# Kernel tuning notes

Hardware: AMD Instinct MI355X
Metric: run time of the kernel (lower is better)

## Reference

```python
import jax, jax.numpy as jnp
import numpy as np

B, N, D = 2, 1024, 1024
H = 4
KD = 512          # key_dim = d_model * 0.5
VD = 1024         # value_dim = d_model
DK = KD // H      # 128 head_qk_dim
DV = VD // H      # 256 head_v_dim
LR = 16           # gate_low_rank_dim
GLN = 16.0        # gate_logit_normalizer
EPS = 1e-5


def setup_inputs() -> dict:
    key = jax.random.key(0)
    ks = jax.random.split(key, 10)
    s = 0.02
    return {
        "x": jax.random.normal(ks[0], (B, N, D), jnp.float32),
        "Wq": jax.random.normal(ks[1], (D, KD), jnp.float32) * s,
        "Wk": jax.random.normal(ks[2], (D, KD), jnp.float32) * s,
        "Wv": jax.random.normal(ks[3], (D, VD), jnp.float32) * s,
        "Wg": jax.random.normal(ks[4], (D, VD), jnp.float32) * s,
        "Wgk1": jax.random.normal(ks[5], (D, LR), jnp.float32) * s,
        "Wgk2": jax.random.normal(ks[6], (LR, KD), jnp.float32) * s,
        "bgk2": jax.random.normal(ks[7], (KD,), jnp.float32) * s,
        "Wout": jax.random.normal(ks[8], (VD, D), jnp.float32) * s,
        "rms_w": jnp.ones((DV,), jnp.float32),
    }


def _split_heads(t, h):
    b, n, hd = t.shape
    return t.reshape(b, n, h, hd // h).transpose(0, 2, 1, 3)  # b h n d


def _gla_scan(q, k, v, g):
    # q,k: [b,h,n,dk]; v: [b,h,n,dv]; g: [b,h,n,dk] (log-decay)
    b, h, n, dk = q.shape
    dv = v.shape[-1]
    qT = jnp.moveaxis(q, 2, 0)  # [n,b,h,dk]
    kT = jnp.moveaxis(k, 2, 0)
    vT = jnp.moveaxis(v, 2, 0)
    gT = jnp.moveaxis(g, 2, 0)

    def step(S, inp):
        qt, kt, vt, gt = inp
        # S_t = diag(exp(g_t)) S_{t-1} + k_t v_t^T ; o_t = q_t S_t
        S = S * jnp.exp(gt)[..., None] + kt[..., None] * vt[..., None, :]
        ot = jnp.einsum('bhk,bhkv->bhv', qt, S)
        return S, ot

    S0 = jnp.zeros((b, h, dk, dv), q.dtype)
    _, o = jax.lax.scan(step, S0, (qT, kT, vT, gT))
    return jnp.moveaxis(o, 0, 2)  # [b,h,n,dv]


def reference(x, Wq, Wk, Wv, Wg, Wgk1, Wgk2, bgk2, Wout, rms_w):
    q = _split_heads(x @ Wq, H)
    k = _split_heads(x @ Wk, H)
    v = _split_heads(x @ Wv, H)
    g = jax.nn.log_sigmoid((x @ Wgk1) @ Wgk2 + bgk2) / GLN
    g = jnp.maximum(g, -3.0)  # chunk mode clamp
    g = _split_heads(g, H)
    o = _gla_scan(q, k, v, g)               # [b,h,n,dv]
    o = o.transpose(0, 2, 1, 3)             # [b,n,h,dv]
    # RMSNorm over head_v_dim
    o = o * jax.lax.rsqrt(jnp.mean(o * o, axis=-1, keepdims=True) + EPS) * rms_w
    o = o.reshape(o.shape[0], o.shape[1], VD)
    o = o * jax.nn.silu(x @ Wg)
    return o @ Wout
```

## Files before the change

kernel.cpp:

```cpp
#include <hip/hip_runtime.h>
#include <math.h>


typedef __attribute__((ext_vector_type(4))) float vf4;
typedef __attribute__((ext_vector_type(2))) float vf2;
typedef __attribute__((ext_vector_type(4))) unsigned int vu4;
typedef __attribute__((ext_vector_type(8))) short short8;
typedef __attribute__((ext_vector_type(4))) unsigned short us4;

#define DEVI static __device__ __forceinline__
DEVI vf4 vzero() { vf4 x = {0.f, 0.f, 0.f, 0.f}; return x; }

DEVI float bf2f(unsigned int u) {
  union { unsigned int i; float f; } c; c.i = u << 16; return c.f;
}
DEVI unsigned short f2bf(float f) {
  union { float f; unsigned int i; } c; c.f = f;
  unsigned int i = c.i;
  return (unsigned short)((i + 0x7fffu + ((i >> 16) & 1u)) >> 16);
}
DEVI void unpack8(vu4 r, float* f) {
  f[0] = bf2f(r.x & 0xffffu); f[1] = bf2f(r.x >> 16);
  f[2] = bf2f(r.y & 0xffffu); f[3] = bf2f(r.y >> 16);
  f[4] = bf2f(r.z & 0xffffu); f[5] = bf2f(r.z >> 16);
  f[6] = bf2f(r.w & 0xffffu); f[7] = bf2f(r.w >> 16);
}
DEVI vu4 pack8(const float* f) {
  vu4 o;
  o.x = (unsigned int)f2bf(f[0]) | ((unsigned int)f2bf(f[1]) << 16);
  o.y = (unsigned int)f2bf(f[2]) | ((unsigned int)f2bf(f[3]) << 16);
  o.z = (unsigned int)f2bf(f[4]) | ((unsigned int)f2bf(f[5]) << 16);
  o.w = (unsigned int)f2bf(f[6]) | ((unsigned int)f2bf(f[7]) << 16);
  return o;
}

DEVI void gld16(const unsigned short* g, unsigned short* l) {
  __builtin_amdgcn_global_load_lds(
      (const __attribute__((address_space(1))) unsigned int*)g,
      (__attribute__((address_space(3))) unsigned int*)l,
      16, 0, 0);
}

__global__ __launch_bounds__(256)
void wtrans_k(const float* __restrict__ Wq, const float* __restrict__ Wk,
              const float* __restrict__ Wv, const float* __restrict__ Wg,
              const float* __restrict__ Wo,
              unsigned short* __restrict__ wqT, unsigned short* __restrict__ wkT,
              unsigned short* __restrict__ wvT, unsigned short* __restrict__ wgT,
              unsigned short* __restrict__ woT) {
  __shared__ float T[2][64][65];
  const int t = threadIdx.x;
  const int r = t >> 2, s = t & 3;
  float f[2][16];
  const float* srcs[2];
  unsigned short* dsts[2];
#pragma unroll
  for (int i = 0; i < 2; ++i) {
    const int tid = blockIdx.x * 2 + i;
    const float* W; unsigned short* O; int kt, cb, N;
    if (tid < 128)       { W = Wq; O = wqT; N = 512;  kt = tid >> 3;          cb = tid & 7;  }
    else if (tid < 256)  { W = Wk; O = wkT; N = 512;  kt = (tid - 128) >> 3;  cb = tid & 7;  }
    else if (tid < 512)  { W = Wv; O = wvT; N = 1024; kt = (tid - 256) >> 4;  cb = tid & 15; }
    else if (tid < 768)  { W = Wg; O = wgT; N = 1024; kt = (tid - 512) >> 4;  cb = tid & 15; }
    else                 { W = Wo; O = woT; N = 1024; kt = (tid - 768) >> 4;  cb = tid & 15; }
    srcs[i] = W + (size_t)(kt * 64 + r) * N + cb * 64 + s * 16;
    dsts[i] = O + (size_t)(cb * 64 + r) * 1024 + kt * 64 + s * 16;
  }
#pragma unroll
  for (int i = 0; i < 2; ++i)
#pragma unroll
    for (int u = 0; u < 4; ++u)
      *(vf4*)&f[i][u * 4] = *(const vf4*)(srcs[i] + u * 4);
#pragma unroll
  for (int i = 0; i < 2; ++i)
#pragma unroll
    for (int u = 0; u < 16; ++u)
      T[i][r][s * 16 + u] = f[i][u];
  __syncthreads();
#pragma unroll
  for (int i = 0; i < 2; ++i) {
    unsigned int pk[8];
#pragma unroll
    for (int u = 0; u < 8; ++u) {
      unsigned int lo = f2bf(T[i][s * 16 + 2 * u][r]);
      unsigned int hi = f2bf(T[i][s * 16 + 2 * u + 1][r]);
      pk[u] = lo | (hi << 16);
    }
    *(vu4*)dsts[i] = *(vu4*)&pk[0];
    *(vu4*)(dsts[i] + 8) = *(vu4*)&pk[4];
  }
}

__global__ __launch_bounds__(256)
void xcvt_lr_k(const float* __restrict__ X, const float* __restrict__ Wgk1,
               unsigned short* __restrict__ xb, float* __restrict__ xl) {
  const int bid = blockIdx.x, t = threadIdx.x;
  if (bid < 512) {
    const size_t base = (size_t)bid * 4096 + t * 16;
    float f[16];
    *(vf4*)&f[0]  = *(const vf4*)(X + base);
    *(vf4*)&f[4]  = *(const vf4*)(X + base + 4);
    *(vf4*)&f[8]  = *(const vf4*)(X + base + 8);
    *(vf4*)&f[12] = *(const vf4*)(X + base + 12);
    *(vu4*)(xb + base) = pack8(f);
    *(vu4*)(xb + base + 8) = pack8(f + 8);
    return;
  }
  const int w = t >> 6, lane = t & 63;
  const int row = (bid - 512) * 4 + w;
  float acc[16];
#pragma unroll
  for (int c2 = 0; c2 < 16; ++c2) acc[c2] = 0.f;
  const float* xp = X + (size_t)row * 1024 + lane * 16;
  float xv[16];
#pragma unroll
  for (int u = 0; u < 4; ++u)
    *(vf4*)&xv[u * 4] = *(const vf4*)(xp + u * 4);
#pragma unroll
  for (int j = 0; j < 16; ++j) {
    const float* wp = Wgk1 + (size_t)(lane * 16 + j) * 16;
    float wv[16];
#pragma unroll
    for (int u = 0; u < 4; ++u)
      *(vf4*)&wv[u * 4] = *(const vf4*)(wp + u * 4);
#pragma unroll
    for (int c2 = 0; c2 < 16; ++c2) acc[c2] = fmaf(xv[j], wv[c2], acc[c2]);
  }
#pragma unroll
  for (int mm = 1; mm < 64; mm <<= 1) {
#pragma unroll
    for (int c2 = 0; c2 < 16; ++c2) acc[c2] += __shfl_xor(acc[c2], mm, 64);
  }
  if (lane == 0) {
#pragma unroll
    for (int c2 = 0; c2 < 16; ++c2) xl[(size_t)row * 16 + c2] = acc[c2];
  }
}

__global__ __launch_bounds__(256)
void proj_mfma_k(const unsigned short* __restrict__ xb,
                 const unsigned short* __restrict__ wqT, const unsigned short* __restrict__ wkT,
                 const unsigned short* __restrict__ wvT, const unsigned short* __restrict__ wgT,
                 unsigned short* __restrict__ qb, unsigned short* __restrict__ kb,
                 unsigned short* __restrict__ vb, unsigned short* __restrict__ sgb) {
  __shared__ __align__(16) unsigned short As[128 * 64];
  __shared__ __align__(16) unsigned short Bs[128 * 64];
  const int t = threadIdx.x;
  const int m0 = blockIdx.y << 7;
  const int nt = blockIdx.x;
  const unsigned short* WT; int n0; int kind;
  if (nt < 4)       { WT = wqT; n0 = nt << 7;        kind = 0; }
  else if (nt < 8)  { WT = wkT; n0 = (nt - 4) << 7;  kind = 1; }
  else if (nt < 16) { WT = wvT; n0 = (nt - 8) << 7;  kind = 2; }
  else              { WT = wgT; n0 = (nt - 16) << 7; kind = 3; }

  const int w = t >> 6, lane = t & 63;
  const int wm = (w >> 1) << 6, wn = (w & 1) << 6;
  const int qd = lane >> 4, m = lane & 15;
  const int srow = lane >> 3;
  const int scol = ((lane & 7) ^ srow) << 3;

  vf4 acc[4][4];
#pragma unroll
  for (int i = 0; i < 4; ++i)
#pragma unroll
    for (int j = 0; j < 4; ++j) acc[i][j] = vzero();

  for (int k0 = 0; k0 < 1024; k0 += 64) {
    __syncthreads();
#pragma unroll
    for (int cc = 0; cc < 4; ++cc) {
      const int c = (w << 2) + cc;
      const int row = (c << 3) + srow;
      gld16(xb + (size_t)(m0 + row) * 1024 + k0 + scol, (unsigned short*)As + (c << 9));
      gld16(WT + (size_t)(n0 + row) * 1024 + k0 + scol, (unsigned short*)Bs + (c << 9));
    }
    __syncthreads();
#pragma unroll
    for (int ks = 0; ks < 2; ++ks) {
      const int sw = (((ks << 2) + qd) ^ (m & 7)) << 3;
      short8 af[4], bf[4];
#pragma unroll
      for (int i = 0; i < 4; ++i)
        af[i] = *(const short8*)&As[(wm + i * 16 + m) * 64 + sw];
#pragma unroll
      for (int j = 0; j < 4; ++j)
        bf[j] = *(const short8*)&Bs[(wn + j * 16 + m) * 64 + sw];
#pragma unroll
      for (int i = 0; i < 4; ++i)
#pragma unroll
        for (int j = 0; j < 4; ++j)
          acc[i][j] = __builtin_amdgcn_mfma_f32_16x16x32_bf16(af[i], bf[j], acc[i][j], 0, 0, 0);
    }
  }
#pragma unroll
  for (int i = 0; i < 4; ++i) {
#pragma unroll
    for (int j = 0; j < 4; ++j) {
#pragma unroll
      for (int r = 0; r < 4; ++r) {
        const int grow = m0 + wm + i * 16 + qd * 4 + r;
        const int gcol = n0 + wn + j * 16 + m;
        float val = acc[i][j][r];
        if (kind == 0)      qb[(size_t)grow * 512 + gcol] = f2bf(val);
        else if (kind == 1) kb[(size_t)grow * 512 + gcol] = f2bf(val);
        else if (kind == 2) vb[(size_t)grow * 1024 + gcol] = f2bf(val);
        else {
          val = val / (1.f + expf(-val));
          sgb[(size_t)grow * 1024 + gcol] = f2bf(val);
        }
      }
    }
  }
}

__global__ __launch_bounds__(256)
void gate_scan_k(const float* __restrict__ xl, const float* __restrict__ W2,
                 const float* __restrict__ bias,
                 unsigned short* __restrict__ q, unsigned short* __restrict__ k,
                 float* __restrict__ ebtot) {
  const int t = threadIdx.x;
  const int w = t >> 6, lane = t & 63;
  const int wid = blockIdx.x * 4 + w;
  const int kt = wid & 31;
  const int c = (wid >> 5) & 15;
  const int b = wid >> 9;
  const int kbase = kt * 16;
  const size_t rowbase = (size_t)b * 1024 + c * 64;

  const float* xp = xl + (rowbase + lane) * 16;
  float xv[16];
#pragma unroll
  for (int u = 0; u < 4; ++u)
    *(vf4*)&xv[u * 4] = *(const vf4*)(xp + u * 4);

  const size_t a = (rowbase + lane) * 512 + kbase;
  vu4 qr0 = *(const vu4*)(q + a), qr1 = *(const vu4*)(q + a + 8);
  vu4 kr0 = *(const vu4*)(k + a), kr1 = *(const vu4*)(k + a + 8);
  float qf[16], kf[16];
  unpack8(qr0, qf); unpack8(qr1, qf + 8);
  unpack8(kr0, kf); unpack8(kr1, kf + 8);

  float gf[16];
#pragma unroll
  for (int cc = 0; cc < 16; ++cc) {
    const int col = kbase + cc;
    float z = bias[col];
#pragma unroll
    for (int j = 0; j < 16; ++j) z = fmaf(xv[j], W2[j * 512 + col], z);
    float ls = fminf(z, 0.f) - log1pf(expf(-fabsf(z)));
    float g = fmaxf(ls * (1.f / 16.f), -3.f);
#pragma unroll
    for (int d = 1; d < 64; d <<= 1) {
      float up = __shfl_up(g, d, 64);
      if (lane >= d) g += up;
    }
    qf[cc] *= expf(g);
    kf[cc] *= expf(fminf(-g, 80.f));
    gf[cc] = g;
  }
  *(vu4*)(q + a) = pack8(qf);
  *(vu4*)(q + a + 8) = pack8(qf + 8);
  *(vu4*)(k + a) = pack8(kf);
  *(vu4*)(k + a + 8) = pack8(kf + 8);
  if (lane == 63) {
    float* ep = ebtot + ((size_t)b * 16 + c) * 512 + kbase;
#pragma unroll
    for (int cc = 0; cc < 16; ++cc) ep[cc] = expf(gf[cc]);
  }
}

__global__ __launch_bounds__(256)
void intra_kv_k(const unsigned short* __restrict__ q16, const unsigned short* __restrict__ k16,
                const unsigned short* __restrict__ v, float* __restrict__ o,
                unsigned short* __restrict__ ST) {
  __shared__ __align__(16) unsigned short Qs[64 * 136];
  __shared__ __align__(16) unsigned short Ks[64 * 136];
  __shared__ __align__(16) unsigned short Kt[128 * 68];
  __shared__ __align__(16) unsigned short Vt[128 * 68];
  __shared__ __align__(16) unsigned short Asb[64 * 68];
  const int t = threadIdx.x;
  const int vh = blockIdx.x, c = blockIdx.y, bh = blockIdx.z;
  const int b = bh >> 2, h = bh & 3;
  const size_t rowbase = (size_t)b * 1024 + c * 64;

#pragma unroll
  for (int u2 = 0; u2 < 4; ++u2) {
    const int id = t + (u2 << 8);
    const int row = id >> 4, kg = id & 15;
    vu4 rq = *(const vu4*)(q16 + (rowbase + row) * 512 + h * 128 + kg * 8);
    *(vu4*)&Qs[row * 136 + kg * 8] = rq;
    vu4 rk = *(const vu4*)(k16 + (rowbase + row) * 512 + h * 128 + kg * 8);
    *(vu4*)&Ks[row * 136 + kg * 8] = rk;
    const unsigned short* kp = (const unsigned short*)&rk;
#pragma unroll
    for (int u = 0; u < 8; ++u)
      Kt[(kg * 8 + u) * 68 + row] = kp[u];
    vu4 rv = *(const vu4*)(v + (rowbase + row) * 1024 + h * 256 + vh * 128 + kg * 8);
    const unsigned short* vp = (const unsigned short*)&rv;
#pragma unroll
    for (int u = 0; u < 8; ++u)
      Vt[(kg * 8 + u) * 68 + row] = vp[u];
  }
  __syncthreads();

  const int w = t >> 6, lane = t & 63;
  const int qd = lane >> 4, m = lane & 15;

  {
    short8 af[4];
#pragma unroll
    for (int kf = 0; kf < 4; ++kf)
      af[kf] = *(const short8*)&Qs[(w * 16 + m) * 136 + kf * 32 + qd * 8];
    vf4 acc[4];
#pragma unroll
    for (int jt = 0; jt < 4; ++jt) acc[jt] = vzero();
#pragma unroll
    for (int jt = 0; jt < 4; ++jt)
#pragma unroll
      for (int kf = 0; kf < 4; ++kf) {
        short8 bfr = *(const short8*)&Ks[(jt * 16 + m) * 136 + kf * 32 + qd * 8];
        acc[jt] = __builtin_amdgcn_mfma_f32_16x16x32_bf16(af[kf], bfr, acc[jt], 0, 0, 0);
      }
#pragma unroll
    for (int jt = 0; jt < 4; ++jt)
#pragma unroll
      for (int r = 0; r < 4; ++r) {
        const int i = w * 16 + qd * 4 + r;
        const int j = jt * 16 + m;
        Asb[i * 68 + j] = f2bf((j <= i) ? acc[jt][r] : 0.f);
      }
  }
  __syncthreads();

  {
    vf4 acc2[4][2];
#pragma unroll
    for (int mt = 0; mt < 4; ++mt) { acc2[mt][0] = vzero(); acc2[mt][1] = vzero(); }
#pragma unroll
    for (int kf = 0; kf < 2; ++kf) {
      short8 bf0 = *(const short8*)&Vt[(w * 32 + m) * 68 + kf * 32 + qd * 8];
      short8 bf1 = *(const short8*)&Vt[(w * 32 + 16 + m) * 68 + kf * 32 + qd * 8];
#pragma unroll
      for (int mt = 0; mt < 4; ++mt) {
        short8 af = *(const short8*)&Asb[(mt * 16 + m) * 68 + kf * 32 + qd * 8];
        acc2[mt][0] = __builtin_amdgcn_mfma_f32_16x16x32_bf16(af, bf0, acc2[mt][0], 0, 0, 0);
        acc2[mt][1] = __builtin_amdgcn_mfma_f32_16x16x32_bf16(af, bf1, acc2[mt][1], 0, 0, 0);
      }
    }
#pragma unroll
    for (int mt = 0; mt < 4; ++mt)
#pragma unroll
      for (int nt = 0; nt < 2; ++nt)
#pragma unroll
        for (int r = 0; r < 4; ++r) {
          const int i = mt * 16 + qd * 4 + r;
          const int vc = h * 256 + vh * 128 + w * 32 + nt * 16 + m;
          o[(rowbase + i) * 1024 + vc] = acc2[mt][nt][r];
        }
  }

  {
    short8 af3[2][2];
#pragma unroll
    for (int mt = 0; mt < 2; ++mt)
#pragma unroll
      for (int kf = 0; kf < 2; ++kf)
        af3[mt][kf] = *(const short8*)&Vt[(w * 32 + mt * 16 + m) * 68 + kf * 32 + qd * 8];
#pragma unroll
    for (int nt = 0; nt < 8; ++nt) {
      vf4 a0 = vzero(), a1 = vzero();
#pragma unroll
      for (int kf = 0; kf < 2; ++kf) {
        short8 bfr = *(const short8*)&Kt[(nt * 16 + m) * 68 + kf * 32 + qd * 8];
        a0 = __builtin_amdgcn_mfma_f32_16x16x32_bf16(af3[0][kf], bfr, a0, 0, 0, 0);
        a1 = __builtin_amdgcn_mfma_f32_16x16x32_bf16(af3[1][kf], bfr, a1, 0, 0, 0);
      }
      const size_t sbase = (size_t)(bh * 16 + c) * 256 + vh * 128 + w * 32;
#pragma unroll
      for (int r = 0; r < 4; ++r) {
        ST[(sbase + qd * 4 + r) * 128 + nt * 16 + m] = f2bf(a0[r]);
        ST[(sbase + 16 + qd * 4 + r) * 128 + nt * 16 + m] = f2bf(a1[r]);
      }
    }
  }
}

__global__ __launch_bounds__(256)
void state_scan_k(unsigned short* __restrict__ ST, const float* __restrict__ ebtot) {
  const int idx = blockIdx.x * 256 + threadIdx.x;
  const int kgp = idx & 63;
  const int vv = (idx >> 6) & 255;
  const int bh = idx >> 14;
  const int b = bh >> 2, h = bh & 3;
  const size_t pbase = (size_t)bh * (16 * 256 * 128) + (size_t)vv * 128 + kgp * 2;
  const size_t ebase = (size_t)b * (16 * 512) + h * 128 + kgp * 2;

  unsigned int stv[16];
  vf2 ebv[16];
#pragma unroll
  for (int c = 0; c < 16; ++c) {
    stv[c] = *(const unsigned int*)(ST + pbase + (size_t)c * 32768);
    ebv[c] = *(const vf2*)(ebtot + ebase + (size_t)c * 512);
  }
  float s0 = 0.f, s1 = 0.f;
#pragma unroll
  for (int c = 0; c < 16; ++c) {
    const float kv0 = bf2f(stv[c] & 0xffffu);
    const float kv1 = bf2f(stv[c] >> 16);
    const unsigned int outw =
        (unsigned int)f2bf(s0) | ((unsigned int)f2bf(s1) << 16);
    *(unsigned int*)(ST + pbase + (size_t)c * 32768) = outw;
    s0 = (s0 + kv0) * ebv[c].x;
    s1 = (s1 + kv1) * ebv[c].y;
  }
}

__global__ __launch_bounds__(256)
void o_inter_k(const unsigned short* __restrict__ q16, const unsigned short* __restrict__ ST,
               float* __restrict__ o) {
  __shared__ __align__(16) unsigned short Qs[64 * 136];
  __shared__ __align__(16) unsigned short Ss[128 * 136];
  const int t = threadIdx.x;
  const int vt = blockIdx.x, c = blockIdx.y, bh = blockIdx.z;
  const int b = bh >> 2, h = bh & 3;
  const size_t rowbase = (size_t)b * 1024 + c * 64;

#pragma unroll
  for (int u2 = 0; u2 < 4; ++u2) {
    const int id = t + (u2 << 8);
    const int row = id >> 4, kg = id & 15;
    *(vu4*)&Qs[row * 136 + kg * 8] =
        *(const vu4*)(q16 + (rowbase + row) * 512 + h * 128 + kg * 8);
  }
#pragma unroll
  for (int u2 = 0; u2 < 8; ++u2) {
    const int id = t + (u2 << 8);
    const int vrow = id >> 4, kg = id & 15;
    *(vu4*)&Ss[vrow * 136 + kg * 8] =
        *(const vu4*)(ST + ((size_t)(bh * 16 + c) * 256 + vt * 128 + vrow) * 128 + kg * 8);
  }
  __syncthreads();

  const int w = t >> 6, lane = t & 63;
  const int qd = lane >> 4, m = lane & 15;
  short8 af[4];
#pragma unroll
  for (int kf = 0; kf < 4; ++kf)
    af[kf] = *(const short8*)&Qs[(w * 16 + m) * 136 + kf * 32 + qd * 8];
#pragma unroll
  for (int nt = 0; nt < 8; ++nt) {
    vf4 acc = vzero();
#pragma unroll
    for (int kf = 0; kf < 4; ++kf) {
      short8 bfr = *(const short8*)&Ss[(nt * 16 + m) * 136 + kf * 32 + qd * 8];
      acc = __builtin_amdgcn_mfma_f32_16x16x32_bf16(af[kf], bfr, acc, 0, 0, 0);
    }
    float* base = o + (rowbase + w * 16 + qd * 4) * 1024 + h * 256 + vt * 128 + nt * 16 + m;
#pragma unroll
    for (int r = 0; r < 4; ++r)
      base[(size_t)r * 1024] += acc[r];
  }
}

__global__ __launch_bounds__(256)
void norm_gate_k(const float* __restrict__ o, const float* __restrict__ rmsw,
                 const unsigned short* __restrict__ sg,
                 unsigned short* __restrict__ ob) {
  const int t = threadIdx.x;
  const int w = t >> 6, lane = t & 63;
  const int grp = blockIdx.x * 4 + w;
  const int row = grp >> 2, h = grp & 3;
  const size_t base = (size_t)row * 1024 + h * 256 + lane * 4;
  vf4 val = *(const vf4*)(o + base);
  float ss = val.x * val.x + val.y * val.y + val.z * val.z + val.w * val.w;
#pragma unroll
  for (int mm = 1; mm < 64; mm <<= 1) ss += __shfl_xor(ss, mm, 64);
  const float scale = rsqrtf(ss * (1.f / 256.f) + 1e-5f);
  us4 sgv = *(const us4*)(sg + base);
  vf4 rw = *(const vf4*)(rmsw + lane * 4);
  us4 outv;
  outv.x = f2bf(val.x * scale * rw.x * bf2f((unsigned int)sgv.x));
  outv.y = f2bf(val.y * scale * rw.y * bf2f((unsigned int)sgv.y));
  outv.z = f2bf(val.z * scale * rw.z * bf2f((unsigned int)sgv.z));
  outv.w = f2bf(val.w * scale * rw.w * bf2f((unsigned int)sgv.w));
  *(us4*)(ob + base) = outv;
}

__global__ __launch_bounds__(256)
void out_mfma_k(const unsigned short* __restrict__ Ab,
                const unsigned short* __restrict__ woT, float* __restrict__ Y) {
  __shared__ __align__(16) unsigned short As[64 * 64];
  __shared__ __align__(16) unsigned short Bs[128 * 64];
  const int t = threadIdx.x;
  const int m0 = blockIdx.y << 6;
  const int n0 = blockIdx.x << 7;
  const int w = t >> 6, lane = t & 63;
  const int wm = (w >> 1) * 32, wn = (w & 1) * 64;
  const int qd = lane >> 4, m = lane & 15;
  const int srow = lane >> 3;
  const int scol = ((lane & 7) ^ srow) << 3;

  vf4 acc[2][4];
#pragma unroll
  for (int i = 0; i < 2; ++i)
#pragma unroll
    for (int j = 0; j < 4; ++j) acc[i][j] = vzero();

  for (int k0 = 0; k0 < 1024; k0 += 64) {
    __syncthreads();
#pragma unroll
    for (int cc = 0; cc < 2; ++cc) {
      const int c = (w << 1) + cc;
      const int row = (c << 3) + srow;
      gld16(Ab + (size_t)(m0 + row) * 1024 + k0 + scol, (unsigned short*)As + (c << 9));
    }
#pragma unroll
    for (int cc = 0; cc < 4; ++cc) {
      const int c = (w << 2) + cc;
      const int row = (c << 3) + srow;
      gld16(woT + (size_t)(n0 + row) * 1024 + k0 + scol, (unsigned short*)Bs + (c << 9));
    }
    __syncthreads();
#pragma unroll
    for (int ks = 0; ks < 2; ++ks) {
      const int sw = (((ks << 2) + qd) ^ (m & 7)) << 3;
      short8 af[2], bf[4];
#pragma unroll
      for (int i = 0; i < 2; ++i)
        af[i] = *(const short8*)&As[(wm + i * 16 + m) * 64 + sw];
#pragma unroll
      for (int j = 0; j < 4; ++j)
        bf[j] = *(const short8*)&Bs[(wn + j * 16 + m) * 64 + sw];
#pragma unroll
      for (int i = 0; i < 2; ++i)
#pragma unroll
        for (int j = 0; j < 4; ++j)
          acc[i][j] = __builtin_amdgcn_mfma_f32_16x16x32_bf16(af[i], bf[j], acc[i][j], 0, 0, 0);
    }
  }
#pragma unroll
  for (int i = 0; i < 2; ++i)
#pragma unroll
    for (int j = 0; j < 4; ++j)
#pragma unroll
      for (int r = 0; r < 4; ++r) {
        const int grow = m0 + wm + i * 16 + qd * 4 + r;
        const int gcol = n0 + wn + j * 16 + m;
        Y[(size_t)grow * 1024 + gcol] = acc[i][j][r];
      }
}

extern "C" void kernel_launch(void* const* d_in, const int* in_sizes, int n_in,
                              void* d_out, int out_size, void* d_ws, size_t ws_size,
                              hipStream_t stream) {
  const float* x    = (const float*)d_in[0];
  const float* Wq   = (const float*)d_in[1];
  const float* Wk   = (const float*)d_in[2];
  const float* Wv   = (const float*)d_in[3];
  const float* Wg   = (const float*)d_in[4];
  const float* Wgk1 = (const float*)d_in[5];
  const float* Wgk2 = (const float*)d_in[6];
  const float* bgk2 = (const float*)d_in[7];
  const float* Wout = (const float*)d_in[8];
  const float* rmsw = (const float*)d_in[9];

  const size_t MB = 1u << 20;
  char* w = (char*)d_ws;
  unsigned short* qb16   = (unsigned short*)(w);
  unsigned short* kb16   = (unsigned short*)(w + 2 * MB);
  unsigned short* vbuf   = (unsigned short*)(w + 4 * MB);
  unsigned short* sgbuf  = (unsigned short*)(w + 8 * MB);
  float*          obuf   = (float*)(w + 12 * MB);
  char*           sreg   = w + 20 * MB;
  unsigned short* xb     = (unsigned short*)sreg;
  unsigned short* STbuf  = (unsigned short*)sreg;
  unsigned short* obuf_b = (unsigned short*)sreg;
  float*          xlbuf  = (float*)(w + 28 * MB);
  float*          ebbuf  = (float*)(w + 28 * MB + 131072);
  unsigned short* wqT    = (unsigned short*)(w + 29 * MB);
  unsigned short* wkT    = (unsigned short*)(w + 30 * MB);
  unsigned short* wvT    = (unsigned short*)(w + 31 * MB);
  unsigned short* wgT    = (unsigned short*)(w + 33 * MB);
  unsigned short* woT    = (unsigned short*)(w + 35 * MB);

  wtrans_k<<<512, 256, 0, stream>>>(Wq, Wk, Wv, Wg, Wout, wqT, wkT, wvT, wgT, woT);
  xcvt_lr_k<<<1024, 256, 0, stream>>>(x, Wgk1, xb, xlbuf);
  proj_mfma_k<<<dim3(24, 16), 256, 0, stream>>>(xb, wqT, wkT, wvT, wgT, qb16, kb16, vbuf, sgbuf);
  gate_scan_k<<<256, 256, 0, stream>>>(xlbuf, Wgk2, bgk2, qb16, kb16, ebbuf);
  intra_kv_k<<<dim3(2, 16, 8), 256, 0, stream>>>(qb16, kb16, vbuf, obuf, STbuf);
  state_scan_k<<<512, 256, 0, stream>>>(STbuf, ebbuf);
  o_inter_k<<<dim3(2, 16, 8), 256, 0, stream>>>(qb16, STbuf, obuf);
  norm_gate_k<<<2048, 256, 0, stream>>>(obuf, rmsw, sgbuf, obuf_b);
  out_mfma_k<<<dim3(8, 32), 256, 0, stream>>>(obuf_b, woT, (float*)d_out);
}
```

Measured before the change: 187.5 us.

## Fuse gate computation into chunk kernels and merge prep launches

Merges the weight-transpose and x-convert/low-rank kernels into a single prep launch. Removes the separate gate_scan kernel by recomputing the gate cumsum and q/k scaling inside intra_kv_k and o_inter_k, so scaled q/k no longer round-trip through global memory. The cost is redundant gate computation: each intra block (two v-halves) and each o_inter block recompute log-sigmoid, the prefix scan and exp per column. This trades two launches and one memory pass for extra ALU work.

Result: slower. 209.0 us (+11.5%).

```diff
diff --git a/kernel.cpp b/kernel.cpp
--- a/kernel.cpp
+++ b/kernel.cpp
@@ -41,22 +41,86 @@
       16, 0, 0);
 }
 
+DEVI float gate_g(const float* xv, const float* __restrict__ W2,
+                  const float* __restrict__ bias, int col, int lane) {
+  float z = bias[col];
+#pragma unroll
+  for (int j = 0; j < 16; ++j) z = fmaf(xv[j], W2[j * 512 + col], z);
+  float ls = fminf(z, 0.f) - log1pf(expf(-fabsf(z)));
+  float g = fmaxf(ls * (1.f / 16.f), -3.f);
+#pragma unroll
+  for (int d = 1; d < 64; d <<= 1) {
+    float up = __shfl_up(g, d, 64);
+    if (lane >= d) g += up;
+  }
+  return g;
+}
+
 __global__ __launch_bounds__(256)
-void wtrans_k(const float* __restrict__ Wq, const float* __restrict__ Wk,
-              const float* __restrict__ Wv, const float* __restrict__ Wg,
-              const float* __restrict__ Wo,
-              unsigned short* __restrict__ wqT, unsigned short* __restrict__ wkT,
-              unsigned short* __restrict__ wvT, unsigned short* __restrict__ wgT,
-              unsigned short* __restrict__ woT) {
+void prep_k(const float* __restrict__ Wq, const float* __restrict__ Wk,
+            const float* __restrict__ Wv, const float* __restrict__ Wg,
+            const float* __restrict__ Wo, const float* __restrict__ X,
+            const float* __restrict__ Wgk1,
+            unsigned short* __restrict__ wqT, unsigned short* __restrict__ wkT,
+            unsigned short* __restrict__ wvT, unsigned short* __restrict__ wgT,
+            unsigned short* __restrict__ woT, unsigned short* __restrict__ xb,
+            float* __restrict__ xl) {
   __shared__ float T[2][64][65];
+  const int bid = blockIdx.x;
   const int t = threadIdx.x;
+
+  if (bid >= 1024) {
+    const int w = t >> 6, lane = t & 63;
+    const int row = (bid - 1024) * 4 + w;
+    float acc[16];
+#pragma unroll
+    for (int c2 = 0; c2 < 16; ++c2) acc[c2] = 0.f;
+    const float* xp = X + (size_t)row * 1024 + lane * 16;
+    float xv[16];
+#pragma unroll
+    for (int u = 0; u < 4; ++u)
+      *(vf4*)&xv[u * 4] = *(const vf4*)(xp + u * 4);
+#pragma unroll
+    for (int j = 0; j < 16; ++j) {
+      const float* wp = Wgk1 + (size_t)(lane * 16 + j) * 16;
+      float wv[16];
+#pragma unroll
+      for (int u = 0; u < 4; ++u)
+        *(vf4*)&wv[u * 4] = *(const vf4*)(wp + u * 4);
+#pragma unroll
+      for (int c2 = 0; c2 < 16; ++c2) acc[c2] = fmaf(xv[j], wv[c2], acc[c2]);
+    }
+#pragma unroll
+    for (int mm = 1; mm < 64; mm <<= 1) {
+#pragma unroll
+      for (int c2 = 0; c2 < 16; ++c2) acc[c2] += __shfl_xor(acc[c2], mm, 64);
+    }
+    if (lane == 0) {
+#pragma unroll
+      for (int c2 = 0; c2 < 16; ++c2) xl[(size_t)row * 16 + c2] = acc[c2];
+    }
+    return;
+  }
+
+  if (bid >= 512) {
+    const size_t base = (size_t)(bid - 512) * 4096 + t * 16;
+    float f[16];
+    *(vf4*)&f[0]  = *(const vf4*)(X + base);
+    *(vf4*)&f[4]  = *(const vf4*)(X + base + 4);
+    *(vf4*)&f[8]  = *(const vf4*)(X + base + 8);
+    *(vf4*)&f[12] = *(const vf4*)(X + base + 12);
+    *(vu4*)(xb + base) = pack8(f);
+    *(vu4*)(xb + base + 8) = pack8(f + 8);
+    return;
+  }
+
   const int r = t >> 2, s = t & 3;
   float f[2][16];
   const float* srcs[2];
   unsigned short* dsts[2];
 #pragma unroll
   for (int i = 0; i < 2; ++i) {
-    const int tid = blockIdx.x * 2 + i;
+    const int tid = bid * 2 + i;
     const float* W; unsigned short* O; int kt, cb, N;
     if (tid < 128)       { W = Wq; O = wqT; N = 512;  kt = tid >> 3;          cb = tid & 7;  }
     else if (tid < 256)  { W = Wk; O = wkT; N = 512;  kt = (tid - 128) >> 3;  cb = tid & 7;  }
@@ -88,52 +152,6 @@
     }
     *(vu4*)dsts[i] = *(vu4*)&pk[0];
     *(vu4*)(dsts[i] + 8) = *(vu4*)&pk[4];
-  }
-}
-
-__global__ __launch_bounds__(256)
-void xcvt_lr_k(const float* __restrict__ X, const float* __restrict__ Wgk1,
-               unsigned short* __restrict__ xb, float* __restrict__ xl) {
-  const int bid = blockIdx.x, t = threadIdx.x;
-  if (bid < 512) {
-    const size_t base = (size_t)bid * 4096 + t * 16;
-    float f[16];
-    *(vf4*)&f[0]  = *(const vf4*)(X + base);
-    *(vf4*)&f[4]  = *(const vf4*)(X + base + 4);
-    *(vf4*)&f[8]  = *(const vf4*)(X + base + 8);
-    *(vf4*)&f[12] = *(const vf4*)(X + base + 12);
-    *(vu4*)(xb + base) = pack8(f);
-    *(vu4*)(xb + base + 8) = pack8(f + 8);
-    return;
-  }
-  const int w = t >> 6, lane = t & 63;
-  const int row = (bid - 512) * 4 + w;
-  float acc[16];
-#pragma unroll
-  for (int c2 = 0; c2 < 16; ++c2) acc[c2] = 0.f;
-  const float* xp = X + (size_t)row * 1024 + lane * 16;
-  float xv[16];
-#pragma unroll
-  for (int u = 0; u < 4; ++u)
-    *(vf4*)&xv[u * 4] = *(const vf4*)(xp + u * 4);
-#pragma unroll
-  for (int j = 0; j < 16; ++j) {
-    const float* wp = Wgk1 + (size_t)(lane * 16 + j) * 16;
-    float wv[16];
-#pragma unroll
-    for (int u = 0; u < 4; ++u)
-      *(vf4*)&wv[u * 4] = *(const vf4*)(wp + u * 4);
-#pragma unroll
-    for (int c2 = 0; c2 < 16; ++c2) acc[c2] = fmaf(xv[j], wv[c2], acc[c2]);
-  }
-#pragma unroll
-  for (int mm = 1; mm < 64; mm <<= 1) {
-#pragma unroll
-    for (int c2 = 0; c2 < 16; ++c2) acc[c2] += __shfl_xor(acc[c2], mm, 64);
-  }
-  if (lane == 0) {
-#pragma unroll
-    for (int c2 = 0; c2 < 16; ++c2) xl[(size_t)row * 16 + c2] = acc[c2];
   }
 }
 
@@ -215,65 +233,11 @@
 }
 
 __global__ __launch_bounds__(256)
-void gate_scan_k(const float* __restrict__ xl, const float* __restrict__ W2,
-                 const float* __restrict__ bias,
-                 unsigned short* __restrict__ q, unsigned short* __restrict__ k,
-                 float* __restrict__ ebtot) {
-  const int t = threadIdx.x;
-  const int w = t >> 6, lane = t & 63;
-  const int wid = blockIdx.x * 4 + w;
-  const int kt = wid & 31;
-  const int c = (wid >> 5) & 15;
-  const int b = wid >> 9;
-  const int kbase = kt * 16;
-  const size_t rowbase = (size_t)b * 1024 + c * 64;
-
-  const float* xp = xl + (rowbase + lane) * 16;
-  float xv[16];
-#pragma unroll
-  for (int u = 0; u < 4; ++u)
-    *(vf4*)&xv[u * 4] = *(const vf4*)(xp + u * 4);
-
-  const size_t a = (rowbase + lane) * 512 + kbase;
-  vu4 qr0 = *(const vu4*)(q + a), qr1 = *(const vu4*)(q + a + 8);
-  vu4 kr0 = *(const vu4*)(k + a), kr1 = *(const vu4*)(k + a + 8);
-  float qf[16], kf[16];
-  unpack8(qr0, qf); unpack8(qr1, qf + 8);
-  unpack8(kr0, kf); unpack8(kr1, kf + 8);
-
-  float gf[16];
-#pragma unroll
-  for (int cc = 0; cc < 16; ++cc) {
-    const int col = kbase + cc;
-    float z = bias[col];
-#pragma unroll
-    for (int j = 0; j < 16; ++j) z = fmaf(xv[j], W2[j * 512 + col], z);
-    float ls = fminf(z, 0.f) - log1pf(expf(-fabsf(z)));
-    float g = fmaxf(ls * (1.f / 16.f), -3.f);
-#pragma unroll
-    for (int d = 1; d < 64; d <<= 1) {
-      float up = __shfl_up(g, d, 64);
-      if (lane >= d) g += up;
-    }
-    qf[cc] *= expf(g);
-    kf[cc] *= expf(fminf(-g, 80.f));
-    gf[cc] = g;
-  }
-  *(vu4*)(q + a) = pack8(qf);
-  *(vu4*)(q + a + 8) = pack8(qf + 8);
-  *(vu4*)(k + a) = pack8(kf);
-  *(vu4*)(k + a + 8) = pack8(kf + 8);
-  if (lane == 63) {
-    float* ep = ebtot + ((size_t)b * 16 + c) * 512 + kbase;
-#pragma unroll
-    for (int cc = 0; cc < 16; ++cc) ep[cc] = expf(gf[cc]);
-  }
-}
-
-__global__ __launch_bounds__(256)
-void intra_kv_k(const unsigned short* __restrict__ q16, const unsigned short* __restrict__ k16,
+void intra_kv_k(const float* __restrict__ xl, const float* __restrict__ W2,
+                const float* __restrict__ bias,
+                const unsigned short* __restrict__ q16, const unsigned short* __restrict__ k16,
                 const unsigned short* __restrict__ v, float* __restrict__ o,
-                unsigned short* __restrict__ ST) {
+                unsigned short* __restrict__ ST, float* __restrict__ ebtot) {
   __shared__ __align__(16) unsigned short Qs[64 * 136];
   __shared__ __align__(16) unsigned short Ks[64 * 136];
   __shared__ __align__(16) unsigned short Kt[128 * 68];
@@ -283,29 +247,61 @@
   const int vh = blockIdx.x, c = blockIdx.y, bh = blockIdx.z;
   const int b = bh >> 2, h = bh & 3;
   const size_t rowbase = (size_t)b * 1024 + c * 64;
+  const int w = t >> 6, lane = t & 63;
+  const int qd = lane >> 4, m = lane & 15;
 
 #pragma unroll
   for (int u2 = 0; u2 < 4; ++u2) {
     const int id = t + (u2 << 8);
     const int row = id >> 4, kg = id & 15;
-    vu4 rq = *(const vu4*)(q16 + (rowbase + row) * 512 + h * 128 + kg * 8);
-    *(vu4*)&Qs[row * 136 + kg * 8] = rq;
-    vu4 rk = *(const vu4*)(k16 + (rowbase + row) * 512 + h * 128 + kg * 8);
-    *(vu4*)&Ks[row * 136 + kg * 8] = rk;
-    const unsigned short* kp = (const unsigned short*)&rk;
-#pragma unroll
-    for (int u = 0; u < 8; ++u)
-      Kt[(kg * 8 + u) * 68 + row] = kp[u];
     vu4 rv = *(const vu4*)(v + (rowbase + row) * 1024 + h * 256 + vh * 128 + kg * 8);
     const unsigned short* vp = (const unsigned short*)&rv;
 #pragma unroll
     for (int u = 0; u < 8; ++u)
       Vt[(kg * 8 + u) * 68 + row] = vp[u];
   }
+
+  {
+    const float* xp = xl + (rowbase + lane) * 16;
+    float xv[16];
+#pragma unroll
+    for (int u = 0; u < 4; ++u)
+      *(vf4*)&xv[u * 4] = *(const vf4*)(xp + u * 4);
+    const size_t qa = (rowbase + lane) * 512 + h * 128 + w * 32;
+    vu4 rq[4], rk[4];
+#pragma unroll
+    for (int g8 = 0; g8 < 4; ++g8) {
+      rq[g8] = *(const vu4*)(q16 + qa + g8 * 8);
+      rk[g8] = *(const vu4*)(k16 + qa + g8 * 8);
+    }
+#pragma unroll
+    for (int g8 = 0; g8 < 4; ++g8) {
+      float qf[8], kf[8], eqv[8];
+      unpack8(rq[g8], qf); unpack8(rk[g8], kf);
+#pragma unroll
+      for (int cc = 0; cc < 8; ++cc) {
+        const int col = h * 128 + w * 32 + g8 * 8 + cc;
+        float g = gate_g(xv, W2, bias, col, lane);
+        float eq = expf(g);
+        qf[cc] *= eq;
+        kf[cc] *= expf(fminf(-g, 80.f));
+        eqv[cc] = eq;
+      }
+      vu4 pq = pack8(qf), pk4 = pack8(kf);
+      *(vu4*)&Qs[lane * 136 + w * 32 + g8 * 8] = pq;
+      *(vu4*)&Ks[lane * 136 + w * 32 + g8 * 8] = pk4;
+      const unsigned short* kp = (const unsigned short*)&pk4;
+#pragma unroll
+      for (int u = 0; u < 8; ++u)
+        Kt[(w * 32 + g8 * 8 + u) * 68 + lane] = kp[u];
+      if (vh == 0 && lane == 63) {
+        float* ep = ebtot + ((size_t)b * 16 + c) * 512 + h * 128 + w * 32 + g8 * 8;
+#pragma unroll
+        for (int cc = 0; cc < 8; ++cc) ep[cc] = eqv[cc];
+      }
+    }
+  }
   __syncthreads();
-
-  const int w = t >> 6, lane = t & 63;
-  const int qd = lane >> 4, m = lane & 15;
 
   {
     short8 af[4];
@@ -417,22 +413,19 @@
 }
 
 __global__ __launch_bounds__(256)
-void o_inter_k(const unsigned short* __restrict__ q16, const unsigned short* __restrict__ ST,
-               float* __restrict__ o) {
+void o_inter_k(const float* __restrict__ xl, const float* __restrict__ W2,
+               const float* __restrict__ bias,
+               const unsigned short* __restrict__ q16,
+               const unsigned short* __restrict__ ST, float* __restrict__ o) {
   __shared__ __align__(16) unsigned short Qs[64 * 136];
   __shared__ __align__(16) unsigned short Ss[128 * 136];
   const int t = threadIdx.x;
   const int vt = blockIdx.x, c = blockIdx.y, bh = blockIdx.z;
   const int b = bh >> 2, h = bh & 3;
   const size_t rowbase = (size_t)b * 1024 + c * 64;
-
-#pragma unroll
-  for (int u2 = 0; u2 < 4; ++u2) {
-    const int id = t + (u2 << 8);
-    const int row = id >> 4, kg = id & 15;
-    *(vu4*)&Qs[row * 136 + kg * 8] =
-        *(const vu4*)(q16 + (rowbase + row) * 512 + h * 128 + kg * 8);
-  }
+  const int w = t >> 6, lane = t & 63;
+  const int qd = lane >> 4, m = lane & 15;
+
 #pragma unroll
   for (int u2 = 0; u2 < 8; ++u2) {
     const int id = t + (u2 << 8);
@@ -440,10 +433,33 @@
     *(vu4*)&Ss[vrow * 136 + kg * 8] =
         *(const vu4*)(ST + ((size_t)(bh * 16 + c) * 256 + vt * 128 + vrow) * 128 + kg * 8);
   }
+
+  {
+    const float* xp = xl + (rowbase + lane) * 16;
+    float xv[16];
+#pragma unroll
+    for (int u = 0; u < 4; ++u)
+      *(vf4*)&xv[u * 4] = *(const vf4*)(xp + u * 4);
+    const size_t qa = (rowbase + lane) * 512 + h * 128 + w * 32;
+    vu4 rq[4];
+#pragma unroll
+    for (int g8 = 0; g8 < 4; ++g8)
+      rq[g8] = *(const vu4*)(q16 + qa + g8 * 8);
+#pragma unroll
+    for (int g8 = 0; g8 < 4; ++g8) {
+      float qf[8];
+      unpack8(rq[g8], qf);
+#pragma unroll
+      for (int cc = 0; cc < 8; ++cc) {
+        const int col = h * 128 + w * 32 + g8 * 8 + cc;
+        float g = gate_g(xv, W2, bias, col, lane);
+        qf[cc] *= expf(g);
+      }
+      *(vu4*)&Qs[lane * 136 + w * 32 + g8 * 8] = pack8(qf);
+    }
+  }
   __syncthreads();
 
-  const int w = t >> 6, lane = t & 63;
-  const int qd = lane >> 4, m = lane & 15;
   short8 af[4];
 #pragma unroll
   for (int kf = 0; kf < 4; ++kf)
@@ -584,13 +600,13 @@
   unsigned short* wgT    = (unsigned short*)(w + 33 * MB);
   unsigned short* woT    = (unsigned short*)(w + 35 * MB);
 
-  wtrans_k<<<512, 256, 0, stream>>>(Wq, Wk, Wv, Wg, Wout, wqT, wkT, wvT, wgT, woT);
-  xcvt_lr_k<<<1024, 256, 0, stream>>>(x, Wgk1, xb, xlbuf);
+  prep_k<<<1536, 256, 0, stream>>>(Wq, Wk, Wv, Wg, Wout, x, Wgk1,
+                                   wqT, wkT, wvT, wgT, woT, xb, xlbuf);
   proj_mfma_k<<<dim3(24, 16), 256, 0, stream>>>(xb, wqT, wkT, wvT, wgT, qb16, kb16, vbuf, sgbuf);
-  gate_scan_k<<<256, 256, 0, stream>>>(xlbuf, Wgk2, bgk2, qb16, kb16, ebbuf);
-  intra_kv_k<<<dim3(2, 16, 8), 256, 0, stream>>>(qb16, kb16, vbuf, obuf, STbuf);
+  intra_kv_k<<<dim3(2, 16, 8), 256, 0, stream>>>(xlbuf, Wgk2, bgk2, qb16, kb16, vbuf,
+                                                 obuf, STbuf, ebbuf);
   state_scan_k<<<512, 256, 0, stream>>>(STbuf, ebbuf);
-  o_inter_k<<<dim3(2, 16, 8), 256, 0, stream>>>(qb16, STbuf, obuf);
+  o_inter_k<<<dim3(2, 16, 8), 256, 0, stream>>>(xlbuf, Wgk2, bgk2, qb16, STbuf, obuf);
   norm_gate_k<<<2048, 256, 0, stream>>>(obuf, rmsw, sgbuf, obuf_b);
   out_mfma_k<<<dim3(8, 32), 256, 0, stream>>>(obuf_b, woT, (float*)d_out);
 }
```
